# Kernel tuning notes

Hardware: AMD Instinct MI355X
Metric: run time of the kernel (lower is better)

Reference implementation:

```python
import jax, jax.numpy as jnp
import numpy as np

N_NODES = 100000
N_EDGES = 1600000
D_IN = 128
D_HID = 128
GARMENT_SIZE = 80000


def setup_inputs() -> dict:
    key = jax.random.key(0)
    k1, k2, k3, k4, k5, k6 = jax.random.split(key, 6)
    notes = jax.random.normal(k1, (N_NODES, D_IN), dtype=jnp.float32)
    w = jax.random.normal(k2, (D_IN, D_HID), dtype=jnp.float32) * 0.05
    b = jax.random.normal(k3, (D_HID,), dtype=jnp.float32) * 0.05
    edge_src = jax.random.randint(k4, (N_EDGES,), 0, N_NODES, dtype=jnp.int32)
    edge_dst = jax.random.randint(k5, (N_EDGES,), 0, N_NODES, dtype=jnp.int32)
    edge_w = jax.random.uniform(k6, (N_EDGES,), dtype=jnp.float32)
    return {
        "notes": notes,
        "w": w,
        "b": b,
        "edge_src": edge_src,
        "edge_dst": edge_dst,
        "edge_w": edge_w,
        "garment_size": GARMENT_SIZE,
    }


def reference(notes, w, b, edge_src, edge_dst, edge_w, garment_size):
    # Dense projection: X0 = notes @ w   -> [N, H]
    X0 = jnp.einsum("nd,dh->nh", notes, w)
    # edge_convolution_template(edge_function=lambda x, y: y, reduction='weighted'):
    # X1[i] = sum over edges (i -> j) of a_ij * X0[j]
    msgs = X0[edge_dst] * edge_w[:, None]                      # [E, H] gather + scale
    X1 = jax.ops.segment_sum(msgs, edge_src, num_segments=notes.shape[0])  # [N, H]
    X = X1 + b
    # concat(act(X), X0[garment_size:]) along node axis -> [2N - garment_size, H]
    return jnp.concatenate([jax.nn.relu(X), X0[garment_size:]], axis=0)
```

## Files before the change

### kernel.cpp

```cpp
#include <hip/hip_runtime.h>

#define H 128
#define NPB 256
#define NB_MAX 1024
#define FILL_CH 4096

static __device__ __forceinline__ unsigned short f2bf(float f) {
  unsigned u = __float_as_uint(f);
  u += 0x7FFFu + ((u >> 16) & 1u);
  return (unsigned short)(u >> 16);
}

__global__ __launch_bounds__(256) void gemm_kernel(
    const float* __restrict__ notes, const float* __restrict__ w,
    const int* __restrict__ g_ptr, unsigned short* __restrict__ x0h,
    float* __restrict__ out, int* __restrict__ bucketCount, int nb,
    int n_nodes) {
  __shared__ float wtile[32 * H];
  __shared__ float ntile[64 * 32];
  const int tid = threadIdx.x;
  const int tx = tid & 31;
  const int ty = tid >> 5;
  const int rowBlk = blockIdx.x * 64;
  const int g = *g_ptr;

  if (blockIdx.x == 0) {
    for (int i = tid; i < nb; i += 256) bucketCount[i] = 0;
  }

  float acc[8][4];
#pragma unroll
  for (int i = 0; i < 8; ++i)
#pragma unroll
    for (int j = 0; j < 4; ++j) acc[i][j] = 0.f;

  for (int kc = 0; kc < H; kc += 32) {
    __syncthreads();
    {
      const float4* wg = (const float4*)(w + (size_t)kc * H);
      float4* wl = (float4*)wtile;
#pragma unroll
      for (int i = 0; i < 4; ++i) wl[tid + i * 256] = wg[tid + i * 256];
    }
    {
      float4* nl = (float4*)ntile;
#pragma unroll
      for (int i = 0; i < 2; ++i) {
        const int idx = tid + i * 256;
        const int row = idx >> 3;
        const int q = idx & 7;
        const int rr = min(rowBlk + row, n_nodes - 1);
        nl[idx] = *(const float4*)(notes + (size_t)rr * H + kc + q * 4);
      }
    }
    __syncthreads();
#pragma unroll 8
    for (int kk = 0; kk < 32; ++kk) {
      const float4 b4 = *(const float4*)&wtile[kk * H + tx * 4];
      float a[8];
#pragma unroll
      for (int i = 0; i < 8; ++i) a[i] = ntile[(ty * 8 + i) * 32 + kk];
#pragma unroll
      for (int i = 0; i < 8; ++i) {
        acc[i][0] += a[i] * b4.x;
        acc[i][1] += a[i] * b4.y;
        acc[i][2] += a[i] * b4.z;
        acc[i][3] += a[i] * b4.w;
      }
    }
  }

#pragma unroll
  for (int i = 0; i < 8; ++i) {
    const int r = rowBlk + ty * 8 + i;
    if (r < n_nodes) {
      ushort4 h;
      h.x = f2bf(acc[i][0]);
      h.y = f2bf(acc[i][1]);
      h.z = f2bf(acc[i][2]);
      h.w = f2bf(acc[i][3]);
      *(ushort4*)(x0h + (size_t)r * H + tx * 4) = h;
      if (r >= g) {
        float4 v;
        v.x = acc[i][0]; v.y = acc[i][1]; v.z = acc[i][2]; v.w = acc[i][3];
        *(float4*)(out + (size_t)(n_nodes + r - g) * H + tx * 4) = v;
      }
    }
  }
}

__global__ __launch_bounds__(256) void bucket_count_kernel(
    const int* __restrict__ esrc, int* __restrict__ bucketCount, int n_edges,
    int nb) {
  __shared__ int cnt[NB_MAX];
  for (int i = threadIdx.x; i < nb; i += 256) cnt[i] = 0;
  __syncthreads();
  int i = blockIdx.x * 256 + threadIdx.x;
  const int stride = gridDim.x * 256;
  for (; i < n_edges; i += stride) atomicAdd(&cnt[esrc[i] >> 8], 1);
  __syncthreads();
  for (int j = threadIdx.x; j < nb; j += 256) {
    const int c = cnt[j];
    if (c) atomicAdd(&bucketCount[j], c);
  }
}

__global__ __launch_bounds__(256) void bucket_scan_kernel(
    const int* __restrict__ bucketCount, int* __restrict__ bucketBase,
    int* __restrict__ bucketCursor, int* __restrict__ off, int nb,
    int n_nodes, int n_edges) {
  __shared__ int part[256];
  const int t = threadIdx.x;
  const int K = (nb + 255) / 256;
  const int lo = t * K;
  const int hi = min(lo + K, nb);
  int sum = 0;
  for (int i = lo; i < hi; ++i) sum += bucketCount[i];
  part[t] = sum;
  __syncthreads();
  for (int o = 1; o < 256; o <<= 1) {
    const int tv = (t >= o) ? part[t - o] : 0;
    __syncthreads();
    part[t] += tv;
    __syncthreads();
  }
  int run = (t == 0) ? 0 : part[t - 1];
  for (int i = lo; i < hi; ++i) {
    bucketBase[i] = run;
    bucketCursor[i] = run;
    run += bucketCount[i];
  }
  if (t == 255) {
    bucketBase[nb] = part[255];
    off[n_nodes] = n_edges;
  }
}

__global__ __launch_bounds__(256) void bucket_fill_kernel(
    const int* __restrict__ esrc, const int* __restrict__ edst,
    const float* __restrict__ ew, int* __restrict__ bucketCursor,
    int2* __restrict__ sedge, unsigned char* __restrict__ srcloc, int n_edges,
    int nb) {
  __shared__ int2 stage[FILL_CH];
  __shared__ unsigned short bkt16[FILL_CH];
  __shared__ unsigned char loc8[FILL_CH];
  __shared__ int cntA[NB_MAX];
  __shared__ int lbase[NB_MAX];
  __shared__ int cntC[NB_MAX];
  const int t = threadIdx.x;
  const int base = blockIdx.x * FILL_CH;
  const int edgesInBlock = min(FILL_CH, n_edges - base);

  for (int i = t; i < nb; i += 256) {
    cntA[i] = 0;
    cntC[i] = 0;
  }
  __syncthreads();

  for (int k = 0; k < FILL_CH / 256; ++k) {
    const int e = base + k * 256 + t;
    if (e < n_edges) atomicAdd(&cntA[esrc[e] >> 8], 1);
  }
  __syncthreads();

  {
    __shared__ int part[256];
    const int K = (nb + 255) / 256;
    const int lo = t * K;
    const int hi = min(lo + K, nb);
    int sum = 0;
    for (int i = lo; i < hi; ++i) sum += cntA[i];
    part[t] = sum;
    __syncthreads();
    for (int o = 1; o < 256; o <<= 1) {
      const int tv = (t >= o) ? part[t - o] : 0;
      __syncthreads();
      part[t] += tv;
      __syncthreads();
    }
    int run = (t == 0) ? 0 : part[t - 1];
    for (int i = lo; i < hi; ++i) {
      lbase[i] = run;
      run += cntA[i];
    }
  }
  __syncthreads();
  for (int i = t; i < nb; i += 256) {
    const int c = cntA[i];
    cntA[i] = c ? atomicAdd(&bucketCursor[i], c) : 0;
  }
  __syncthreads();

  for (int k = 0; k < FILL_CH / 256; ++k) {
    const int e = base + k * 256 + t;
    if (e < n_edges) {
      const int s = esrc[e];
      const int b = s >> 8;
      const int r = atomicAdd(&cntC[b], 1);
      const int sp = lbase[b] + r;
      int2 pk;
      pk.x = edst[e];
      pk.y = __float_as_int(ew[e]);
      stage[sp] = pk;
      bkt16[sp] = (unsigned short)b;
      loc8[sp] = (unsigned char)(s & 255);
    }
  }
  __syncthreads();

  for (int j = t; j < edgesInBlock; j += 256) {
    const int b = bkt16[j];
    const int pos = cntA[b] + (j - lbase[b]);
    sedge[pos] = stage[j];
    srcloc[pos] = loc8[j];
  }
}

__global__ __launch_bounds__(256) void bucket_sort_kernel(
    const int* __restrict__ bucketBase, const int2* __restrict__ sedge,
    const unsigned char* __restrict__ srcloc, int2* __restrict__ sedge2,
    int* __restrict__ off, int n_nodes) {
  __shared__ int cnt[NPB];
  __shared__ int nodeOff[NPB];
  const int t = threadIdx.x;
  const int beg = bucketBase[blockIdx.x];
  const int end = bucketBase[blockIdx.x + 1];
  const int nodeBase = blockIdx.x * NPB;
  const int nodesInBucket = min(NPB, n_nodes - nodeBase);

  cnt[t] = 0;
  __syncthreads();
  for (int j = beg + t; j < end; j += 256) atomicAdd(&cnt[srcloc[j]], 1);
  __syncthreads();
  {
    const int v = cnt[t];
    nodeOff[t] = v;
    __syncthreads();
    for (int o = 1; o < 256; o <<= 1) {
      const int tv = (t >= o) ? nodeOff[t - o] : 0;
      __syncthreads();
      nodeOff[t] += tv;
      __syncthreads();
    }
    nodeOff[t] -= v;
  }
  if (t < nodesInBucket) off[nodeBase + t] = beg + nodeOff[t];
  cnt[t] = 0;
  __syncthreads();
  for (int j = beg + t; j < end; j += 256) {
    const int loc = srcloc[j];
    const int r = atomicAdd(&cnt[loc], 1);
    sedge2[beg + nodeOff[loc] + r] = sedge[j];
  }
}

__global__ __launch_bounds__(256) void gather_kernel(
    const int* __restrict__ off, const int2* __restrict__ sedge,
    const unsigned short* __restrict__ x0h, const float* __restrict__ b,
    float* __restrict__ out, int n_nodes) {
  const int wave = blockIdx.x * (blockDim.x >> 6) + (threadIdx.x >> 6);
  const int lane = threadIdx.x & 63;
  const int half = lane >> 5;
  const int l32 = lane & 31;
  const int node = wave * 2 + half;
  const bool valid = (node < n_nodes);

  int begH = 0, endH = 0;
  if (valid) {
    begH = off[node];
    endH = off[node + 1];
  }
  const int degH = endH - begH;
  int kmax = max(degH, __shfl_xor(degH, 32));
  const int lastH = max(endH - 1, 0);

  const unsigned* __restrict__ x0u = (const unsigned*)x0h;

  float4 a[4];
#pragma unroll
  for (int j = 0; j < 4; ++j) a[j] = make_float4(0.f, 0.f, 0.f, 0.f);

  for (int k = 0; k < kmax; k += 4) {
    int2 m[4];
#pragma unroll
    for (int j = 0; j < 4; ++j) m[j] = sedge[min(begH + k + j, lastH)];
    uint2 u[4];
#pragma unroll
    for (int j = 0; j < 4; ++j)
      u[j] = *(const uint2*)(x0u + (size_t)m[j].x * 64 + l32 * 2);
#pragma unroll
    for (int j = 0; j < 4; ++j) {
      const float wv = (k + j < degH) ? __int_as_float(m[j].y) : 0.f;
      a[j].x += __uint_as_float(u[j].x << 16) * wv;
      a[j].y += __uint_as_float(u[j].x & 0xFFFF0000u) * wv;
      a[j].z += __uint_as_float(u[j].y << 16) * wv;
      a[j].w += __uint_as_float(u[j].y & 0xFFFF0000u) * wv;
    }
  }

  const float4 bb = ((const float4*)b)[l32];
  float4 r;
  r.x = fmaxf(a[0].x + a[1].x + a[2].x + a[3].x + bb.x, 0.f);
  r.y = fmaxf(a[0].y + a[1].y + a[2].y + a[3].y + bb.y, 0.f);
  r.z = fmaxf(a[0].z + a[1].z + a[2].z + a[3].z + bb.z, 0.f);
  r.w = fmaxf(a[0].w + a[1].w + a[2].w + a[3].w + bb.w, 0.f);
  if (valid) ((float4*)out)[(size_t)node * 32 + l32] = r;
}

__global__ __launch_bounds__(256) void scatter_kernel(
    const int* __restrict__ esrc, const int* __restrict__ edst,
    const float* __restrict__ ew, const unsigned short* __restrict__ x0h,
    float* __restrict__ acc, int n_edges) {
  const int lane = threadIdx.x & 63;
  const int waveId = blockIdx.x * (blockDim.x >> 6) + (threadIdx.x >> 6);
  const int nWaves = gridDim.x * (blockDim.x >> 6);
  const unsigned* __restrict__ x0u = (const unsigned*)x0h;
  for (int e = waveId; e < n_edges; e += nWaves) {
    const int s = esrc[e];
    const int d = edst[e];
    const float wt = ew[e];
    const unsigned u = x0u[(size_t)d * 64 + lane];
    float* p = acc + (size_t)s * H + lane * 2;
    atomicAdd(p, __uint_as_float(u << 16) * wt);
    atomicAdd(p + 1, __uint_as_float(u & 0xFFFF0000u) * wt);
  }
}

__global__ __launch_bounds__(256) void epilogue_kernel(
    float* __restrict__ out, const float* __restrict__ b, int n4) {
  const int i = blockIdx.x * blockDim.x + threadIdx.x;
  if (i >= n4) return;
  float4* o4 = (float4*)out;
  const float4* b4 = (const float4*)b;
  float4 v = o4[i];
  const float4 bb = b4[i & 31];
  v.x = fmaxf(v.x + bb.x, 0.f);
  v.y = fmaxf(v.y + bb.y, 0.f);
  v.z = fmaxf(v.z + bb.z, 0.f);
  v.w = fmaxf(v.w + bb.w, 0.f);
  o4[i] = v;
}

extern "C" void kernel_launch(void* const* d_in, const int* in_sizes, int n_in,
                              void* d_out, int out_size, void* d_ws, size_t ws_size,
                              hipStream_t stream) {
  const float* notes = (const float*)d_in[0];
  const float* w     = (const float*)d_in[1];
  const float* b     = (const float*)d_in[2];
  const int*   esrc  = (const int*)d_in[3];
  const int*   edst  = (const int*)d_in[4];
  const float* ew    = (const float*)d_in[5];
  const int*   gptr  = (const int*)d_in[6];

  const int n_nodes = in_sizes[0] / H;
  const int n_edges = in_sizes[3];
  float* out = (float*)d_out;

  const int nb = (n_nodes + NPB - 1) / NPB;

  char* ws = (char*)d_ws;
  size_t p = 0;
  auto alloc = [&](size_t bytes) -> char* {
    char* cur = ws + p;
    p = (p + bytes + 255) & ~(size_t)255;
    return cur;
  };
  unsigned short* x0h = (unsigned short*)alloc((size_t)n_nodes * H * 2);
  int*  bucketCount  = (int*)alloc((size_t)nb * sizeof(int));
  int*  bucketBase   = (int*)alloc(((size_t)nb + 1) * sizeof(int));
  int*  bucketCursor = (int*)alloc((size_t)nb * sizeof(int));
  int*  off          = (int*)alloc(((size_t)n_nodes + 1) * sizeof(int));
  int2* sedge        = (int2*)alloc((size_t)n_edges * sizeof(int2));
  int2* sedge2       = (int2*)alloc((size_t)n_edges * sizeof(int2));
  unsigned char* srcloc = (unsigned char*)alloc((size_t)n_edges);
  const bool ok = (p <= ws_size) && (nb <= NB_MAX);

  gemm_kernel<<<(n_nodes + 63) / 64, 256, 0, stream>>>(
      notes, w, gptr, x0h, out, bucketCount, ok ? nb : 0, n_nodes);

  if (ok) {
    bucket_count_kernel<<<256, 256, 0, stream>>>(esrc, bucketCount, n_edges,
                                                 nb);
    bucket_scan_kernel<<<1, 256, 0, stream>>>(bucketCount, bucketBase,
                                              bucketCursor, off, nb, n_nodes,
                                              n_edges);
    bucket_fill_kernel<<<(n_edges + FILL_CH - 1) / FILL_CH, 256, 0, stream>>>(
        esrc, edst, ew, bucketCursor, sedge, srcloc, n_edges, nb);
    bucket_sort_kernel<<<nb, 256, 0, stream>>>(bucketBase, sedge, srcloc,
                                               sedge2, off, n_nodes);
    const int waves = (n_nodes + 1) / 2;
    gather_kernel<<<(waves + 3) / 4, 256, 0, stream>>>(off, sedge2, x0h, b,
                                                       out, n_nodes);
  } else {
    hipMemsetAsync(d_out, 0, (size_t)n_nodes * H * sizeof(float), stream);
    scatter_kernel<<<2048, 256, 0, stream>>>(esrc, edst, ew, x0h, out, n_edges);
    const int n4 = n_nodes * H / 4;
    epilogue_kernel<<<(n4 + 255) / 256, 256, 0, stream>>>(out, b, n4);
  }
}
```

Baseline: 291.3 us.

## Fuse bucket counting into GEMM launch and add unclamped fast path in gather

```diff
diff --git a/kernel.cpp b/kernel.cpp
--- a/kernel.cpp
+++ b/kernel.cpp
@@ -4,6 +4,7 @@
 #define NPB 256
 #define NB_MAX 1024
 #define FILL_CH 4096
+#define CNT_BLOCKS 256
 
 static __device__ __forceinline__ unsigned short f2bf(float f) {
   unsigned u = __float_as_uint(f);
@@ -11,22 +12,35 @@
   return (unsigned short)(u >> 16);
 }
 
-__global__ __launch_bounds__(256) void gemm_kernel(
+__global__ __launch_bounds__(256) void gemm_count_kernel(
     const float* __restrict__ notes, const float* __restrict__ w,
-    const int* __restrict__ g_ptr, unsigned short* __restrict__ x0h,
-    float* __restrict__ out, int* __restrict__ bucketCount, int nb,
-    int n_nodes) {
+    const int* __restrict__ g_ptr, const int* __restrict__ esrc,
+    unsigned short* __restrict__ x0h, float* __restrict__ out,
+    int* __restrict__ bucketCount, int nb, int n_nodes, int n_edges,
+    int cntBlocks) {
   __shared__ float wtile[32 * H];
   __shared__ float ntile[64 * 32];
   const int tid = threadIdx.x;
+
+  if (blockIdx.x < cntBlocks) {
+    int* cnt = (int*)wtile;
+    for (int i = tid; i < nb; i += 256) cnt[i] = 0;
+    __syncthreads();
+    int i = blockIdx.x * 256 + tid;
+    const int stride = cntBlocks * 256;
+    for (; i < n_edges; i += stride) atomicAdd(&cnt[esrc[i] >> 8], 1);
+    __syncthreads();
+    for (int j = tid; j < nb; j += 256) {
+      const int c = cnt[j];
+      if (c) atomicAdd(&bucketCount[j], c);
+    }
+    return;
+  }
+
   const int tx = tid & 31;
   const int ty = tid >> 5;
-  const int rowBlk = blockIdx.x * 64;
+  const int rowBlk = (blockIdx.x - cntBlocks) * 64;
   const int g = *g_ptr;
-
-  if (blockIdx.x == 0) {
-    for (int i = tid; i < nb; i += 256) bucketCount[i] = 0;
-  }
 
   float acc[8][4];
 #pragma unroll
@@ -89,22 +103,6 @@
   }
 }
 
-__global__ __launch_bounds__(256) void bucket_count_kernel(
-    const int* __restrict__ esrc, int* __restrict__ bucketCount, int n_edges,
-    int nb) {
-  __shared__ int cnt[NB_MAX];
-  for (int i = threadIdx.x; i < nb; i += 256) cnt[i] = 0;
-  __syncthreads();
-  int i = blockIdx.x * 256 + threadIdx.x;
-  const int stride = gridDim.x * 256;
-  for (; i < n_edges; i += stride) atomicAdd(&cnt[esrc[i] >> 8], 1);
-  __syncthreads();
-  for (int j = threadIdx.x; j < nb; j += 256) {
-    const int c = cnt[j];
-    if (c) atomicAdd(&bucketCount[j], c);
-  }
-}
-
 __global__ __launch_bounds__(256) void bucket_scan_kernel(
     const int* __restrict__ bucketCount, int* __restrict__ bucketBase,
     int* __restrict__ bucketCursor, int* __restrict__ off, int nb,
@@ -271,8 +269,12 @@
     endH = off[node + 1];
   }
   const int degH = endH - begH;
-  int kmax = max(degH, __shfl_xor(degH, 32));
+  const int degO = __shfl_xor(degH, 32);
+  const int kmin = min(degH, degO);
+  const int kmax = max(degH, degO);
+  const int kfull = kmin & ~3;
   const int lastH = max(endH - 1, 0);
+  const int2* __restrict__ sp = sedge + begH;
 
   const unsigned* __restrict__ x0u = (const unsigned*)x0h;
 
@@ -280,7 +282,25 @@
 #pragma unroll
   for (int j = 0; j < 4; ++j) a[j] = make_float4(0.f, 0.f, 0.f, 0.f);
 
-  for (int k = 0; k < kmax; k += 4) {
+  int k = 0;
+  for (; k < kfull; k += 4) {
+    int2 m[4];
+#pragma unroll
+    for (int j = 0; j < 4; ++j) m[j] = sp[k + j];
+    uint2 u[4];
+#pragma unroll
+    for (int j = 0; j < 4; ++j)
+      u[j] = *(const uint2*)(x0u + (size_t)m[j].x * 64 + l32 * 2);
+#pragma unroll
+    for (int j = 0; j < 4; ++j) {
+      const float wv = __int_as_float(m[j].y);
+      a[j].x += __uint_as_float(u[j].x << 16) * wv;
+      a[j].y += __uint_as_float(u[j].x & 0xFFFF0000u) * wv;
+      a[j].z += __uint_as_float(u[j].y << 16) * wv;
+      a[j].w += __uint_as_float(u[j].y & 0xFFFF0000u) * wv;
+    }
+  }
+  for (; k < kmax; k += 4) {
     int2 m[4];
 #pragma unroll
     for (int j = 0; j < 4; ++j) m[j] = sedge[min(begH + k + j, lastH)];
@@ -375,12 +395,13 @@
   unsigned char* srcloc = (unsigned char*)alloc((size_t)n_edges);
   const bool ok = (p <= ws_size) && (nb <= NB_MAX);
 
-  gemm_kernel<<<(n_nodes + 63) / 64, 256, 0, stream>>>(
-      notes, w, gptr, x0h, out, bucketCount, ok ? nb : 0, n_nodes);
+  const int gemmBlocks = (n_nodes + 63) / 64;
 
   if (ok) {
-    bucket_count_kernel<<<256, 256, 0, stream>>>(esrc, bucketCount, n_edges,
-                                                 nb);
+    hipMemsetAsync(bucketCount, 0, (size_t)nb * sizeof(int), stream);
+    gemm_count_kernel<<<gemmBlocks + CNT_BLOCKS, 256, 0, stream>>>(
+        notes, w, gptr, esrc, x0h, out, bucketCount, nb, n_nodes, n_edges,
+        CNT_BLOCKS);
     bucket_scan_kernel<<<1, 256, 0, stream>>>(bucketCount, bucketBase,
                                               bucketCursor, off, nb, n_nodes,
                                               n_edges);
@@ -392,6 +413,8 @@
     gather_kernel<<<(waves + 3) / 4, 256, 0, stream>>>(off, sedge2, x0h, b,
                                                        out, n_nodes);
   } else {
+    gemm_count_kernel<<<gemmBlocks, 256, 0, stream>>>(
+        notes, w, gptr, esrc, x0h, out, bucketCount, 0, n_nodes, n_edges, 0);
     hipMemsetAsync(d_out, 0, (size_t)n_nodes * H * sizeof(float), stream);
     scatter_kernel<<<2048, 256, 0, stream>>>(esrc, edst, ew, x0h, out, n_edges);
     const int n4 = n_nodes * H / 4;
```

Measured after the change: 280.2 us. 1.04x faster.
